# Optimization experiments

Hardware: AMD Instinct MI355X
Metric: run time of the kernel (lower is better)

The kernel has to match this reference:

```python
import jax, jax.numpy as jnp
import numpy as np

B, S, D = 1, 2048, 2048
HQ, HKV, HD = 32, 4, 128
E, K, F = 8, 2, 768
EPS = 1e-6
ROPE_THETA = 1000000.0


def rmsnorm(x, scale, eps=EPS):
    var = jnp.mean(jnp.square(x), axis=-1, keepdims=True)
    return x * jax.lax.rsqrt(var + eps) * scale


def rotate_half(x):
    h = x.shape[-1] // 2
    return jnp.concatenate([-x[..., h:], x[..., :h]], axis=-1)


def rope_cos_sin(seq_len, head_dim, dtype=jnp.float32):
    inv_freq = 1.0 / (ROPE_THETA ** (jnp.arange(0, head_dim, 2, dtype=jnp.float32) / head_dim))
    angles = jnp.arange(seq_len, dtype=jnp.float32)[:, None] * inv_freq[None, :]  # (S, HD/2)
    emb = jnp.concatenate([angles, angles], axis=-1)  # (S, HD)
    return jnp.cos(emb).astype(dtype), jnp.sin(emb).astype(dtype)


def setup_inputs() -> dict:
    key = jax.random.key(0)
    ks = jax.random.split(key, 16)
    s = lambda i, shape, scale: jax.random.normal(ks[i], shape, dtype=jnp.float32) * scale
    inp = {
        "hidden_states": s(0, (B, S, D), 1.0),
        "ln1_scale": jnp.ones((D,), jnp.float32),
        "ln2_scale": jnp.ones((D,), jnp.float32),
        "Wq": s(1, (D, HQ * HD), 0.02),
        "Wk": s(2, (D, HKV * HD), 0.02),
        "Wv": s(3, (D, HKV * HD), 0.02),
        "Wo": s(4, (HQ * HD, D), 0.02),
        "q_norm_scale": jnp.ones((HD,), jnp.float32),
        "k_norm_scale": jnp.ones((HD,), jnp.float32),
        "router_W": s(5, (D, E), 0.02),
        "up_W": s(6, (E, D, F), 0.02),
        "up_b": jnp.zeros((E, F), jnp.float32),
        "down_W": s(7, (E, F, D), 0.02),
        "down_b": jnp.zeros((E, D), jnp.float32),
    }
    return inp


def reference(hidden_states, ln1_scale, ln2_scale, Wq, Wk, Wv, Wo,
              q_norm_scale, k_norm_scale, router_W, up_W, up_b, down_W, down_b):
    b, s_len, d = hidden_states.shape
    # ---- pre-norm + self-attention ----
    residual = hidden_states
    x = rmsnorm(hidden_states, ln1_scale)
    q = (x @ Wq).reshape(b, s_len, HQ, HD)
    k = (x @ Wk).reshape(b, s_len, HKV, HD)
    v = (x @ Wv).reshape(b, s_len, HKV, HD)
    q = rmsnorm(q, q_norm_scale)
    k = rmsnorm(k, k_norm_scale)
    cos, sin = rope_cos_sin(s_len, HD, q.dtype)
    cos = cos[None, :, None, :]
    sin = sin[None, :, None, :]
    q = q * cos + rotate_half(q) * sin
    k = k * cos + rotate_half(k) * sin
    g = HQ // HKV
    k = jnp.repeat(k, g, axis=2)  # (b, s, HQ, HD)
    v = jnp.repeat(v, g, axis=2)
    scores = jnp.einsum('bqhd,bkhd->bhqk', q, k) / jnp.sqrt(jnp.asarray(HD, q.dtype))
    causal = jnp.tril(jnp.ones((s_len, s_len), bool))
    scores = jnp.where(causal[None, None], scores, jnp.asarray(-1e9, scores.dtype))
    probs = jax.nn.softmax(scores, axis=-1)
    attn = jnp.einsum('bhqk,bkhd->bqhd', probs, v).reshape(b, s_len, HQ * HD)
    attn_out = attn @ Wo
    hidden = residual + attn_out
    # ---- pre-norm + dense-all-experts MoE ----
    residual = hidden
    xf = rmsnorm(hidden, ln2_scale).reshape(-1, d)  # (T, D)
    router_logits = xf @ router_W  # (T, E)
    routing_weights = jax.nn.softmax(router_logits, axis=-1)
    gating_weights, selected = jax.lax.top_k(routing_weights, K)  # (T, K)
    gating_weights = gating_weights / jnp.sum(gating_weights, axis=-1, keepdims=True)
    expert_mask = jax.nn.one_hot(selected, E, dtype=gating_weights.dtype)  # (T, K, E)
    h = jax.nn.silu(jnp.einsum('td,edf->tef', xf, up_W) + up_b[None])  # (T, E, F)
    expert_outputs = jnp.einsum('tef,efd->ted', h, down_W) + down_b[None]  # (T, E, D)
    weighted = jnp.einsum('tke,ted->tkd', expert_mask, expert_outputs)  # (T, K, D)
    moe_out = jnp.sum(weighted * gating_weights[..., None], axis=1).reshape(b, s_len, d)
    hidden = residual + moe_out
    # ---- load balancing auxiliary loss (no attention mask path) ----
    expert_usage = jnp.mean(jnp.mean(expert_mask, axis=0), axis=0) * E  # (E,)
    su = jnp.sum(expert_usage)
    aux_loss = su * su / (E * E)
    return hidden, router_logits, aux_loss
```

## Files before the change

kernel.cpp:

```cpp
#include <hip/hip_runtime.h>
#include <cmath>

typedef __bf16 bf16_t;
typedef __bf16 bf16x8 __attribute__((ext_vector_type(8)));
typedef __bf16 bf16x4 __attribute__((ext_vector_type(4)));
typedef float  f32x4  __attribute__((ext_vector_type(4)));

#define SLEN 2048
#define DMOD 2048
#define NHQ  32
#define NHKV 4
#define HD   128
#define NQC  4096
#define NKVC 512
#define NQKVC 5120
#define NEXP 8
#define NF   768

#define KSTR 136
#define VSTR 72
#define PSTR 72

__device__ __forceinline__ float wredsum(float v) {
#pragma unroll
  for (int off = 32; off > 0; off >>= 1) v += __shfl_xor(v, off);
  return v;
}

__device__ __forceinline__ void gll16(const bf16_t* g, bf16_t* l) {
  __builtin_amdgcn_global_load_lds((const __attribute__((address_space(1))) void*)g,
                                   (__attribute__((address_space(3))) void*)l, 16, 0, 0);
}

__global__ void rope_table_k(float* __restrict__ cosT, float* __restrict__ sinT) {
  int idx = blockIdx.x * 256 + threadIdx.x;
  if (idx >= SLEN * 64) return;
  int t = idx >> 6, j = idx & 63;
  double inv = exp(-0.2158673524681918 * (double)j);
  double ang = (double)t * inv;
  cosT[idx] = (float)cos(ang);
  sinT[idx] = (float)sin(ang);
}

__global__ __launch_bounds__(256) void transpose_split2_k(const float* __restrict__ in,
                                                          bf16_t* __restrict__ outH,
                                                          bf16_t* __restrict__ outL,
                                                          int R, int C) {
  __shared__ float tile[32][33];
  int tx = threadIdx.x, ty = threadIdx.y;
  int c0 = blockIdx.x * 32, r0 = blockIdx.y * 32;
#pragma unroll
  for (int i = 0; i < 4; i++)
    tile[ty + i * 8][tx] = in[(size_t)(r0 + ty + i * 8) * C + c0 + tx];
  __syncthreads();
#pragma unroll
  for (int i = 0; i < 4; i++) {
    int c = c0 + ty + i * 8;
    int r = r0 + tx;
    float w = tile[tx][ty + i * 8];
    bf16_t hi = (bf16_t)w;
    bf16_t lo = (bf16_t)(w - (float)hi);
    size_t o = (size_t)c * R + r;
    outH[o] = hi;
    outL[o] = lo;
  }
}

__global__ __launch_bounds__(256) void transpose_plain_k(const float* __restrict__ in,
                                                         bf16_t* __restrict__ out,
                                                         int R, int C) {
  __shared__ float tile[32][33];
  int b = blockIdx.z;
  const float* inb = in + (size_t)b * R * C;
  bf16_t* outb = out + (size_t)b * R * C;
  int tx = threadIdx.x, ty = threadIdx.y;
  int c0 = blockIdx.x * 32, r0 = blockIdx.y * 32;
#pragma unroll
  for (int i = 0; i < 4; i++)
    tile[ty + i * 8][tx] = inb[(size_t)(r0 + ty + i * 8) * C + c0 + tx];
  __syncthreads();
#pragma unroll
  for (int i = 0; i < 4; i++) {
    int c = c0 + ty + i * 8;
    int r = r0 + tx;
    outb[(size_t)c * R + r] = (bf16_t)tile[tx][ty + i * 8];
  }
}

__global__ __launch_bounds__(256) void rmsnorm1_k(const float* __restrict__ hs,
                                                  const float* __restrict__ sc,
                                                  bf16_t* __restrict__ xnH,
                                                  bf16_t* __restrict__ xnL) {
  const int t = blockIdx.x;
  const float* row = hs + (size_t)t * DMOD;
  const int tid = threadIdx.x;
  const int i0 = tid * 8;
  float4 a = *(const float4*)(row + i0);
  float4 b = *(const float4*)(row + i0 + 4);
  float x[8] = {a.x, a.y, a.z, a.w, b.x, b.y, b.z, b.w};
  float ss = 0.f;
#pragma unroll
  for (int j = 0; j < 8; j++) ss += x[j] * x[j];
  ss = wredsum(ss);
  __shared__ float red[4];
  if ((tid & 63) == 0) red[tid >> 6] = ss;
  __syncthreads();
  float rn = rsqrtf((red[0] + red[1] + red[2] + red[3]) * (1.f / 2048.f) + 1e-6f);
#pragma unroll
  for (int j = 0; j < 8; j++) {
    float v = x[j] * rn * sc[i0 + j];
    bf16_t hi = (bf16_t)v;
    bf16_t lo = (bf16_t)(v - (float)hi);
    xnH[(size_t)t * DMOD + i0 + j] = hi;
    xnL[(size_t)t * DMOD + i0 + j] = lo;
  }
}

template <bool RESID>
__global__ __launch_bounds__(256, 3) void gemm_split_k(const bf16_t* __restrict__ Ah,
                                                       const bf16_t* __restrict__ Al,
                                                       int lda,
                                                       const bf16_t* __restrict__ Bh,
                                                       const bf16_t* __restrict__ Bl,
                                                       int ldb, int K,
                                                       const float* __restrict__ resid,
                                                       float* __restrict__ C, int ldc) {
  __shared__ bf16_t AsH[2][128][32], AsL[2][128][32], BsH[2][64][32], BsL[2][64][32];
  const int t = threadIdx.x;
  const int w = t >> 6, lane = t & 63;
  const int m16 = lane & 15, quad = lane >> 4;
  const int nwg = gridDim.x * gridDim.y;
  const int flat = blockIdx.y * gridDim.x + blockIdx.x;
  int tile = flat;
  if ((nwg & 7) == 0) tile = (flat & 7) * (nwg >> 3) + (flat >> 3);
  const int bx = tile % gridDim.x, by = tile / gridDim.x;
  const int m0 = by * 128, n0 = bx * 64;
  const int wm = (w & 1) * 64, wn = (w >> 1) * 32;
  f32x4 acc[4][2];
#pragma unroll
  for (int i = 0; i < 4; i++)
#pragma unroll
    for (int j = 0; j < 2; j++) acc[i][j] = (f32x4){0.f, 0.f, 0.f, 0.f};

  const int srow = t >> 2;
  const int scol = (t & 3) * 8;
  const int lw = w * 512;
  const bf16_t* gAh0 = Ah + (size_t)(m0 + srow) * lda + scol;
  const bf16_t* gAh1 = Ah + (size_t)(m0 + 64 + srow) * lda + scol;
  const bf16_t* gAl0 = Al + (size_t)(m0 + srow) * lda + scol;
  const bf16_t* gAl1 = Al + (size_t)(m0 + 64 + srow) * lda + scol;
  const bf16_t* gBh0 = Bh + (size_t)(n0 + srow) * ldb + scol;
  const bf16_t* gBl0 = Bl + (size_t)(n0 + srow) * ldb + scol;

  auto stage = [&](int buf, int k0) {
    gll16(gAh0 + k0, &AsH[buf][0][0] + lw);
    gll16(gAh1 + k0, &AsH[buf][0][0] + 2048 + lw);
    gll16(gAl0 + k0, &AsL[buf][0][0] + lw);
    gll16(gAl1 + k0, &AsL[buf][0][0] + 2048 + lw);
    gll16(gBh0 + k0, &BsH[buf][0][0] + lw);
    gll16(gBl0 + k0, &BsL[buf][0][0] + lw);
  };

  stage(0, 0);
  int cur = 0;
  for (int k0 = 32; k0 <= K; k0 += 32) {
    if (k0 < K) {
      stage(cur ^ 1, k0);
      asm volatile("s_waitcnt vmcnt(6)" ::: "memory");
    } else {
      asm volatile("s_waitcnt vmcnt(0)" ::: "memory");
    }
    __builtin_amdgcn_sched_barrier(0);
    __builtin_amdgcn_s_barrier();
    __builtin_amdgcn_sched_barrier(0);
    bf16x8 a_h[4], a_l[4];
#pragma unroll
    for (int mt = 0; mt < 4; mt++) {
      a_h[mt] = *(const bf16x8*)(&AsH[cur][wm + mt * 16 + m16][quad * 8]);
      a_l[mt] = *(const bf16x8*)(&AsL[cur][wm + mt * 16 + m16][quad * 8]);
    }
#pragma unroll
    for (int nt = 0; nt < 2; nt++) {
      bf16x8 b_h = *(const bf16x8*)(&BsH[cur][wn + nt * 16 + m16][quad * 8]);
      bf16x8 b_l = *(const bf16x8*)(&BsL[cur][wn + nt * 16 + m16][quad * 8]);
#pragma unroll
      for (int mt = 0; mt < 4; mt++) {
        acc[mt][nt] = __builtin_amdgcn_mfma_f32_16x16x32_bf16(a_h[mt], b_h, acc[mt][nt], 0, 0, 0);
        acc[mt][nt] = __builtin_amdgcn_mfma_f32_16x16x32_bf16(a_l[mt], b_h, acc[mt][nt], 0, 0, 0);
        acc[mt][nt] = __builtin_amdgcn_mfma_f32_16x16x32_bf16(a_h[mt], b_l, acc[mt][nt], 0, 0, 0);
      }
    }
    __builtin_amdgcn_sched_barrier(0);
    __builtin_amdgcn_s_barrier();
    __builtin_amdgcn_sched_barrier(0);
    cur ^= 1;
  }
#pragma unroll
  for (int mt = 0; mt < 4; mt++)
#pragma unroll
    for (int r = 0; r < 4; r++) {
      const size_t row = m0 + wm + mt * 16 + quad * 4 + r;
#pragma unroll
      for (int nt = 0; nt < 2; nt++) {
        const size_t idx = row * ldc + n0 + wn + nt * 16 + m16;
        if (RESID) C[idx] = acc[mt][nt][r] + resid[idx];
        else       C[idx] = acc[mt][nt][r];
      }
    }
}

__global__ __launch_bounds__(128) void qknorm_rope_k(float* __restrict__ qkv,
                                                     const float* __restrict__ qsc,
                                                     const float* __restrict__ ksc,
                                                     const float* __restrict__ cosT,
                                                     const float* __restrict__ sinT) {
  const int t = blockIdx.x;
  const int hh = blockIdx.y;
  const bool isq = hh < NHQ;
  float* ptr = qkv + (size_t)t * NQKVC + (isq ? hh * HD : NQC + (hh - NHQ) * HD);
  const int i = threadIdx.x;
  float x = ptr[i];
  float ss = x * x;
  ss = wredsum(ss);
  __shared__ float red2[2];
  __shared__ float xs[128];
  if ((i & 63) == 0) red2[i >> 6] = ss;
  __syncthreads();
  float rn = rsqrtf((red2[0] + red2[1]) * (1.f / 128.f) + 1e-6f);
  float xn = x * rn * (isq ? qsc[i] : ksc[i]);
  xs[i] = xn;
  __syncthreads();
  int j = i & 63;
  float c = cosT[t * 64 + j];
  float s = sinT[t * 64 + j];
  float rot = (i < 64) ? -xs[i + 64] : xs[i - 64];
  ptr[i] = xn * c + rot * s;
}

__global__ __launch_bounds__(256) void kprep_k(const float* __restrict__ qkv,
                                               bf16_t* __restrict__ Kh,
                                               bf16_t* __restrict__ Kl) {
  const int gid = blockIdx.x * 256 + threadIdx.x;
  const int tok = gid >> 6;
  const int c = (gid & 63) * 8;
  const int hk = c >> 7, d = c & 127;
  const float* p = qkv + (size_t)tok * NQKVC + NQC + c;
  float4 a = *(const float4*)p;
  float4 b = *(const float4*)(p + 4);
  float xv[8] = {a.x, a.y, a.z, a.w, b.x, b.y, b.z, b.w};
  bf16x8 hv, lv;
#pragma unroll
  for (int j = 0; j < 8; j++) {
    bf16_t hi = (bf16_t)xv[j];
    hv[j] = hi;
    lv[j] = (bf16_t)(xv[j] - (float)hi);
  }
  const size_t o = ((size_t)hk * SLEN + tok) * HD + d;
  *(bf16x8*)(Kh + o) = hv;
  *(bf16x8*)(Kl + o) = lv;
}

__global__ __launch_bounds__(256) void vprep_k(const float* __restrict__ qkv,
                                               bf16_t* __restrict__ Vh,
                                               bf16_t* __restrict__ Vl) {
  __shared__ float tile[32][33];
  const int hk = blockIdx.z;
  const int tx = threadIdx.x, ty = threadIdx.y;
  const int t0 = blockIdx.x * 32, d0 = blockIdx.y * 32;
#pragma unroll
  for (int i = 0; i < 4; i++)
    tile[ty + i * 8][tx] =
        qkv[(size_t)(t0 + ty + i * 8) * NQKVC + NQC + NKVC + hk * HD + d0 + tx];
  __syncthreads();
#pragma unroll
  for (int i = 0; i < 4; i++) {
    int d = d0 + ty + i * 8;
    int tk = t0 + tx;
    float wv = tile[tx][ty + i * 8];
    bf16_t hi = (bf16_t)wv;
    size_t o = ((size_t)hk * HD + d) * SLEN + tk;
    Vh[o] = hi;
    Vl[o] = (bf16_t)(wv - (float)hi);
  }
}

__global__ __launch_bounds__(256) void attn_mfma_k(const float* __restrict__ qkv,
                                                   const bf16_t* __restrict__ Kph,
                                                   const bf16_t* __restrict__ Kpl,
                                                   const bf16_t* __restrict__ Vph,
                                                   const bf16_t* __restrict__ Vpl,
                                                   bf16_t* __restrict__ attnH,
                                                   bf16_t* __restrict__ attnL) {
  const int bx = blockIdx.x;
  const int hh = blockIdx.y;
  const int hk = hh >> 3;
  __shared__ bf16_t sK[2][64][KSTR];
  __shared__ bf16_t sV[2][128][VSTR];
  const int t = threadIdx.x;
  const int w = t >> 6, lane = t & 63;
  const int m16 = lane & 15, quad = lane >> 4;
  const float SCALE = 0.08838834764831845f;

  const int ksr = t >> 4;
  const int ksc = (t & 15) * 8;
  const int vsd = t >> 3;
  const int vsk = (t & 7) * 8;
  const bf16_t* KbH = Kph + (size_t)hk * SLEN * HD;
  const bf16_t* KbL = Kpl + (size_t)hk * SLEN * HD;
  const bf16_t* VbH = Vph + (size_t)hk * HD * SLEN;
  const bf16_t* VbL = Vpl + (size_t)hk * HD * SLEN;
  bf16_t* sP = &sK[0][0][0];

  for (int half = 0; half < 2; half++) {
    const int qb = half ? bx : 31 - bx;
    const int qg = qb * 64 + w * 16 + m16;

    bf16x8 Qh[4], Ql[4];
    {
      const int qrow = qb * 64 + w * 16 + m16;
      const float* qp = qkv + (size_t)qrow * NQKVC + hh * HD + quad * 8;
#pragma unroll
      for (int kc = 0; kc < 4; kc++) {
        float4 x0 = *(const float4*)(qp + kc * 32);
        float4 x1 = *(const float4*)(qp + kc * 32 + 4);
        float xv[8] = {x0.x, x0.y, x0.z, x0.w, x1.x, x1.y, x1.z, x1.w};
#pragma unroll
        for (int j = 0; j < 8; j++) {
          bf16_t hi = (bf16_t)xv[j];
          Qh[kc][j] = hi;
          Ql[kc][j] = (bf16_t)(xv[j] - (float)hi);
        }
      }
    }
    f32x4 acc[8];
#pragma unroll
    for (int i = 0; i < 8; i++) acc[i] = (f32x4){0.f, 0.f, 0.f, 0.f};
    float mrow = -1e30f, lrow = 0.f;

    for (int kb = 0; kb <= qb; kb++) {
      __syncthreads();
      {
#pragma unroll
        for (int i = 0; i < 4; i++) {
          const int row = ksr + i * 16;
          const size_t go = (size_t)(kb * 64 + row) * HD + ksc;
          *(bf16x8*)(&sK[0][row][ksc]) = *(const bf16x8*)(KbH + go);
          *(bf16x8*)(&sK[1][row][ksc]) = *(const bf16x8*)(KbL + go);
        }
      }
      {
#pragma unroll
        for (int i = 0; i < 4; i++) {
          const int d = vsd + i * 32;
          const size_t go = (size_t)d * SLEN + kb * 64 + vsk;
          *(bf16x8*)(&sV[0][d][vsk]) = *(const bf16x8*)(VbH + go);
          *(bf16x8*)(&sV[1][d][vsk]) = *(const bf16x8*)(VbL + go);
        }
      }
      __syncthreads();
      f32x4 xs[4];
#pragma unroll
      for (int nt = 0; nt < 4; nt++) {
        f32x4 s = (f32x4){0.f, 0.f, 0.f, 0.f};
        if (kb < qb || nt <= w) {
#pragma unroll
          for (int kc = 0; kc < 4; kc++) {
            bf16x8 kh = *(const bf16x8*)(&sK[0][nt * 16 + m16][kc * 32 + quad * 8]);
            bf16x8 kl = *(const bf16x8*)(&sK[1][nt * 16 + m16][kc * 32 + quad * 8]);
            s = __builtin_amdgcn_mfma_f32_16x16x32_bf16(kh, Qh[kc], s, 0, 0, 0);
            s = __builtin_amdgcn_mfma_f32_16x16x32_bf16(kh, Ql[kc], s, 0, 0, 0);
            s = __builtin_amdgcn_mfma_f32_16x16x32_bf16(kl, Qh[kc], s, 0, 0, 0);
          }
        }
        xs[nt] = s;
      }
      __syncthreads();
      float xr[4][4], p[4][4];
      float mx = -1e30f;
#pragma unroll
      for (int nt = 0; nt < 4; nt++)
#pragma unroll
        for (int r = 0; r < 4; r++) {
          int kvg = kb * 64 + nt * 16 + quad * 4 + r;
          float v = (kvg <= qg) ? xs[nt][r] * SCALE : -1e30f;
          xr[nt][r] = v;
          mx = fmaxf(mx, v);
        }
      mx = fmaxf(mx, __shfl_xor(mx, 16));
      mx = fmaxf(mx, __shfl_xor(mx, 32));
      float mn = fmaxf(mrow, mx);
      float al = __expf(mrow - mn);
      float rs = 0.f;
#pragma unroll
      for (int nt = 0; nt < 4; nt++)
#pragma unroll
        for (int r = 0; r < 4; r++) {
          float pv = __expf(xr[nt][r] - mn);
          p[nt][r] = pv;
          rs += pv;
        }
      rs += __shfl_xor(rs, 16);
      rs += __shfl_xor(rs, 32);
      lrow = lrow * al + rs;
      mrow = mn;
#pragma unroll
      for (int dt = 0; dt < 8; dt++)
#pragma unroll
        for (int r = 0; r < 4; r++) acc[dt][r] *= al;
      {
        bf16_t* base = sP + (size_t)w * 2 * 16 * PSTR;
#pragma unroll
        for (int nt = 0; nt < 4; nt++) {
          bf16x4 hv, lv;
#pragma unroll
          for (int r = 0; r < 4; r++) {
            float pv = p[nt][r];
            bf16_t hi = (bf16_t)pv;
            hv[r] = hi;
            lv[r] = (bf16_t)(pv - (float)hi);
          }
          *(bf16x4*)(base + m16 * PSTR + nt * 16 + quad * 4) = hv;
          *(bf16x4*)(base + 16 * PSTR + m16 * PSTR + nt * 16 + quad * 4) = lv;
        }
      }
      {
        const bf16_t* base = sP + (size_t)w * 2 * 16 * PSTR;
        bf16x8 Ph[2], Pl[2];
#pragma unroll
        for (int kc = 0; kc < 2; kc++) {
          Ph[kc] = *(const bf16x8*)(base + m16 * PSTR + kc * 32 + quad * 8);
          Pl[kc] = *(const bf16x8*)(base + 16 * PSTR + m16 * PSTR + kc * 32 + quad * 8);
        }
#pragma unroll
        for (int dt = 0; dt < 8; dt++)
#pragma unroll
          for (int kc = 0; kc < 2; kc++) {
            bf16x8 vh = *(const bf16x8*)(&sV[0][dt * 16 + m16][kc * 32 + quad * 8]);
            bf16x8 vl = *(const bf16x8*)(&sV[1][dt * 16 + m16][kc * 32 + quad * 8]);
            acc[dt] = __builtin_amdgcn_mfma_f32_16x16x32_bf16(vh, Ph[kc], acc[dt], 0, 0, 0);
            acc[dt] = __builtin_amdgcn_mfma_f32_16x16x32_bf16(vh, Pl[kc], acc[dt], 0, 0, 0);
            acc[dt] = __builtin_amdgcn_mfma_f32_16x16x32_bf16(vl, Ph[kc], acc[dt], 0, 0, 0);
          }
      }
    }
    __syncthreads();
    float* tb = (float*)(&sK[0][0][0]) + (size_t)w * 2048;
    const float linv = 1.f / lrow;
#pragma unroll
    for (int dt = 0; dt < 8; dt++) {
      f32x4 v = acc[dt];
#pragma unroll
      for (int r = 0; r < 4; r++) v[r] *= linv;
      *(f32x4*)(tb + m16 * 128 + dt * 16 + quad * 4) = v;
    }
    __syncthreads();
    {
      const int qr = lane >> 2, c0 = (lane & 3) * 32;
      const int tok = qb * 64 + w * 16 + qr;
      const size_t ro = (size_t)tok * NQC + hh * HD + c0;
#pragma unroll
      for (int j = 0; j < 4; j++) {
        float4 a = *(const float4*)(tb + qr * 128 + c0 + j * 8);
        float4 b = *(const float4*)(tb + qr * 128 + c0 + j * 8 + 4);
        float xv[8] = {a.x, a.y, a.z, a.w, b.x, b.y, b.z, b.w};
        bf16x8 hv, lv;
#pragma unroll
        for (int jj = 0; jj < 8; jj++) {
          bf16_t hi = (bf16_t)xv[jj];
          hv[jj] = hi;
          lv[jj] = (bf16_t)(xv[jj] - (float)hi);
        }
        *(bf16x8*)(attnH + ro + j * 8) = hv;
        *(bf16x8*)(attnL + ro + j * 8) = lv;
      }
    }
  }
}

__global__ __launch_bounds__(256) void rmsnorm2_router_k(const float* __restrict__ hid,
                                                         const float* __restrict__ sc2,
                                                         const float* __restrict__ rW,
                                                         bf16_t* __restrict__ xf,
                                                         float* __restrict__ rlog) {
  const int t = blockIdx.x;
  const float* row = hid + (size_t)t * DMOD;
  const int tid = threadIdx.x;
  const int i0 = tid * 8;
  float4 a = *(const float4*)(row + i0);
  float4 b = *(const float4*)(row + i0 + 4);
  float x[8] = {a.x, a.y, a.z, a.w, b.x, b.y, b.z, b.w};
  float ss = 0.f;
#pragma unroll
  for (int j = 0; j < 8; j++) ss += x[j] * x[j];
  ss = wredsum(ss);
  __shared__ float red[4];
  if ((tid & 63) == 0) red[tid >> 6] = ss;
  __syncthreads();
  float rn = rsqrtf((red[0] + red[1] + red[2] + red[3]) * (1.f / 2048.f) + 1e-6f);
  float acc[8];
#pragma unroll
  for (int e = 0; e < 8; e++) acc[e] = 0.f;
#pragma unroll
  for (int j = 0; j < 8; j++) {
    float xn = x[j] * rn * sc2[i0 + j];
    xf[(size_t)t * DMOD + i0 + j] = (bf16_t)xn;
    const float* w = rW + (size_t)(i0 + j) * NEXP;
#pragma unroll
    for (int e = 0; e < 8; e++) acc[e] += xn * w[e];
  }
#pragma unroll
  for (int e = 0; e < 8; e++) acc[e] = wredsum(acc[e]);
  __shared__ float wacc[4][8];
  if ((tid & 63) == 0)
#pragma unroll
    for (int e = 0; e < 8; e++) wacc[tid >> 6][e] = acc[e];
  __syncthreads();
  if (tid < 8) rlog[t * NEXP + tid] = wacc[0][tid] + wacc[1][tid] + wacc[2][tid] + wacc[3][tid];
}

__global__ void topk_k(const float* __restrict__ rlog, int* __restrict__ sel,
                       float* __restrict__ gates, float* __restrict__ aux) {
  int t = blockIdx.x * 256 + threadIdx.x;
  if (t == 0) aux[0] = 1.0f;
  if (t >= SLEN) return;
  const float* l = rlog + t * NEXP;
  int i1 = 0; float v1 = l[0];
#pragma unroll
  for (int e = 1; e < 8; e++) if (l[e] > v1) { v1 = l[e]; i1 = e; }
  int i2 = -1; float v2 = -1e30f;
#pragma unroll
  for (int e = 0; e < 8; e++) if (e != i1 && l[e] > v2) { v2 = l[e]; i2 = e; }
  float e21 = expf(v2 - v1);
  float inv = 1.f / (1.f + e21);
  sel[t * 2 + 0] = i1;
  sel[t * 2 + 1] = i2;
  gates[t * 2 + 0] = inv;
  gates[t * 2 + 1] = e21 * inv;
}

__global__ void scatter_k(const int* __restrict__ sel, const float* __restrict__ gates,
                          int* __restrict__ cnt, int* __restrict__ tok,
                          float* __restrict__ gateL, int* __restrict__ posOf) {
  int i = blockIdx.x * 256 + threadIdx.x;
  if (i >= SLEN * 2) return;
  int e = sel[i];
  int pos = atomicAdd(&cnt[e], 1);
  tok[e * SLEN + pos] = i >> 1;
  gateL[e * SLEN + pos] = gates[i];
  posOf[i] = pos;
}

__global__ void prefix_k(const int* __restrict__ cnt, int* __restrict__ baseP) {
  if (threadIdx.x == 0) {
    int b = 0;
#pragma unroll
    for (int e = 0; e < 8; e++) { baseP[e] = b; b += cnt[e]; }
  }
}

__global__ __launch_bounds__(256, 5) void gemm_up_k(const bf16_t* __restrict__ xf,
                                                    const bf16_t* __restrict__ upWT,
                                                    const int* __restrict__ cnt,
                                                    const int* __restrict__ tok,
                                                    const float* __restrict__ up_b,
                                                    bf16_t* __restrict__ hbuf) {
  const int e = blockIdx.z;
  const int c = cnt[e];
  const int m0 = blockIdx.y * 128;
  if (m0 >= c) return;
  const int n0 = blockIdx.x * 64;
  __shared__ bf16_t As[2][128][32], Bs[2][64][32];
  const int t = threadIdx.x;
  const int w = t >> 6, lane = t & 63;
  const int m16 = lane & 15, quad = lane >> 4;
  const int wm = (w & 1) * 64, wn = (w >> 1) * 32;
  const int srow = t >> 2, scol = (t & 3) * 8;
  const int lw = w * 512;
  const int* tokE = tok + e * SLEN;
  int r0 = m0 + srow;      if (r0 >= c) r0 = c - 1;
  int r1 = m0 + 64 + srow; if (r1 >= c) r1 = c - 1;
  const bf16_t* ga0 = xf + (size_t)tokE[r0] * DMOD + scol;
  const bf16_t* ga1 = xf + (size_t)tokE[r1] * DMOD + scol;
  const bf16_t* gb0 = upWT + (size_t)e * NF * DMOD + (size_t)(n0 + srow) * DMOD + scol;
  f32x4 acc[4][2];
#pragma unroll
  for (int i = 0; i < 4; i++)
#pragma unroll
    for (int j = 0; j < 2; j++) acc[i][j] = (f32x4){0.f, 0.f, 0.f, 0.f};

  auto stage = [&](int buf, int k0) {
    gll16(ga0 + k0, &As[buf][0][0] + lw);
    gll16(ga1 + k0, &As[buf][0][0] + 2048 + lw);
    gll16(gb0 + k0, &Bs[buf][0][0] + lw);
  };

  stage(0, 0);
  int cur = 0;
  for (int k0 = 32; k0 <= DMOD; k0 += 32) {
    if (k0 < DMOD) {
      stage(cur ^ 1, k0);
      asm volatile("s_waitcnt vmcnt(3)" ::: "memory");
    } else {
      asm volatile("s_waitcnt vmcnt(0)" ::: "memory");
    }
    __builtin_amdgcn_sched_barrier(0);
    __builtin_amdgcn_s_barrier();
    __builtin_amdgcn_sched_barrier(0);
    bf16x8 a[4];
#pragma unroll
    for (int mt = 0; mt < 4; mt++)
      a[mt] = *(const bf16x8*)(&As[cur][wm + mt * 16 + m16][quad * 8]);
#pragma unroll
    for (int nt = 0; nt < 2; nt++) {
      bf16x8 b = *(const bf16x8*)(&Bs[cur][wn + nt * 16 + m16][quad * 8]);
#pragma unroll
      for (int mt = 0; mt < 4; mt++)
        acc[mt][nt] = __builtin_amdgcn_mfma_f32_16x16x32_bf16(a[mt], b, acc[mt][nt], 0, 0, 0);
    }
    __builtin_amdgcn_sched_barrier(0);
    __builtin_amdgcn_s_barrier();
    __builtin_amdgcn_sched_barrier(0);
    cur ^= 1;
  }
#pragma unroll
  for (int mt = 0; mt < 4; mt++)
#pragma unroll
    for (int r = 0; r < 4; r++) {
      int slot = m0 + wm + mt * 16 + quad * 4 + r;
      if (slot < c) {
#pragma unroll
        for (int nt = 0; nt < 2; nt++) {
          int n = n0 + wn + nt * 16 + m16;
          float x = acc[mt][nt][r] + up_b[e * NF + n];
          float v = x / (1.f + __expf(-x));
          hbuf[((size_t)e * SLEN + slot) * NF + n] = (bf16_t)v;
        }
      }
    }
}

__global__ __launch_bounds__(256, 5) void gemm_down_k(const bf16_t* __restrict__ hbuf,
                                                      const bf16_t* __restrict__ downWT,
                                                      const int* __restrict__ cnt,
                                                      const float* __restrict__ gateL,
                                                      const float* __restrict__ down_b,
                                                      const int* __restrict__ baseP,
                                                      float* __restrict__ dbuf) {
  const int e = blockIdx.z;
  const int c = cnt[e];
  const int m0 = blockIdx.y * 128;
  if (m0 >= c) return;
  const int n0 = blockIdx.x * 64;
  __shared__ bf16_t As[2][128][32], Bs[2][64][32];
  const int t = threadIdx.x;
  const int w = t >> 6, lane = t & 63;
  const int m16 = lane & 15, quad = lane >> 4;
  const int wm = (w & 1) * 64, wn = (w >> 1) * 32;
  const int srow = t >> 2, scol = (t & 3) * 8;
  const int lw = w * 512;
  const bf16_t* Ab = hbuf + (size_t)e * SLEN * NF;
  const bf16_t* ga0 = Ab + (size_t)(m0 + srow) * NF + scol;
  const bf16_t* ga1 = Ab + (size_t)(m0 + 64 + srow) * NF + scol;
  const bf16_t* gb0 = downWT + (size_t)e * DMOD * NF + (size_t)(n0 + srow) * NF + scol;
  f32x4 acc[4][2];
#pragma unroll
  for (int i = 0; i < 4; i++)
#pragma unroll
    for (int j = 0; j < 2; j++) acc[i][j] = (f32x4){0.f, 0.f, 0.f, 0.f};

  auto stage = [&](int buf, int k0) {
    gll16(ga0 + k0, &As[buf][0][0] + lw);
    gll16(ga1 + k0, &As[buf][0][0] + 2048 + lw);
    gll16(gb0 + k0, &Bs[buf][0][0] + lw);
  };

  stage(0, 0);
  int cur = 0;
  for (int k0 = 32; k0 <= NF; k0 += 32) {
    if (k0 < NF) {
      stage(cur ^ 1, k0);
      asm volatile("s_waitcnt vmcnt(3)" ::: "memory");
    } else {
      asm volatile("s_waitcnt vmcnt(0)" ::: "memory");
    }
    __builtin_amdgcn_sched_barrier(0);
    __builtin_amdgcn_s_barrier();
    __builtin_amdgcn_sched_barrier(0);
    bf16x8 a[4];
#pragma unroll
    for (int mt = 0; mt < 4; mt++)
      a[mt] = *(const bf16x8*)(&As[cur][wm + mt * 16 + m16][quad * 8]);
#pragma unroll
    for (int nt = 0; nt < 2; nt++) {
      bf16x8 b = *(const bf16x8*)(&Bs[cur][wn + nt * 16 + m16][quad * 8]);
#pragma unroll
      for (int mt = 0; mt < 4; mt++)
        acc[mt][nt] = __builtin_amdgcn_mfma_f32_16x16x32_bf16(a[mt], b, acc[mt][nt], 0, 0, 0);
    }
    __builtin_amdgcn_sched_barrier(0);
    __builtin_amdgcn_s_barrier();
    __builtin_amdgcn_sched_barrier(0);
    cur ^= 1;
  }
  const int eb = baseP[e];
#pragma unroll
  for (int mt = 0; mt < 4; mt++)
#pragma unroll
    for (int r = 0; r < 4; r++) {
      int slot = m0 + wm + mt * 16 + quad * 4 + r;
      if (slot < c) {
        float g = gateL[e * SLEN + slot];
#pragma unroll
        for (int nt = 0; nt < 2; nt++) {
          int n = n0 + wn + nt * 16 + m16;
          dbuf[(size_t)(eb + slot) * DMOD + n] = g * (acc[mt][nt][r] + down_b[e * DMOD + n]);
        }
      }
    }
}

__global__ __launch_bounds__(256) void combine_k(const float* __restrict__ dbuf,
                                                 const int* __restrict__ sel,
                                                 const int* __restrict__ posOf,
                                                 const int* __restrict__ baseP,
                                                 float* __restrict__ dout) {
  const int t = blockIdx.x;
  const int i0 = threadIdx.x * 8;
  const int r0 = baseP[sel[t * 2 + 0]] + posOf[t * 2 + 0];
  const int r1 = baseP[sel[t * 2 + 1]] + posOf[t * 2 + 1];
  const float* a = dbuf + (size_t)r0 * DMOD + i0;
  const float* b = dbuf + (size_t)r1 * DMOD + i0;
  float* o = dout + (size_t)t * DMOD + i0;
  float4 o0 = *(const float4*)o,       o1 = *(const float4*)(o + 4);
  float4 a0 = *(const float4*)a,       a1 = *(const float4*)(a + 4);
  float4 b0 = *(const float4*)b,       b1 = *(const float4*)(b + 4);
  o0.x += a0.x + b0.x; o0.y += a0.y + b0.y; o0.z += a0.z + b0.z; o0.w += a0.w + b0.w;
  o1.x += a1.x + b1.x; o1.y += a1.y + b1.y; o1.z += a1.z + b1.z; o1.w += a1.w + b1.w;
  *(float4*)o = o0;
  *(float4*)(o + 4) = o1;
}

extern "C" void kernel_launch(void* const* d_in, const int* in_sizes, int n_in,
                              void* d_out, int out_size, void* d_ws, size_t ws_size,
                              hipStream_t stream) {
  (void)in_sizes; (void)n_in; (void)out_size;
  const float* hs   = (const float*)d_in[0];
  const float* ln1  = (const float*)d_in[1];
  const float* ln2  = (const float*)d_in[2];
  const float* Wq   = (const float*)d_in[3];
  const float* Wk   = (const float*)d_in[4];
  const float* Wv   = (const float*)d_in[5];
  const float* Wo   = (const float*)d_in[6];
  const float* qns  = (const float*)d_in[7];
  const float* kns  = (const float*)d_in[8];
  const float* rW   = (const float*)d_in[9];
  const float* upW  = (const float*)d_in[10];
  const float* upB  = (const float*)d_in[11];
  const float* dnW  = (const float*)d_in[12];
  const float* dnB  = (const float*)d_in[13];
  float* dout = (float*)d_out;

  const size_t NEED = 135431168ull;
  if (ws_size < NEED) return;
  char* ws = (char*)d_ws;
  const size_t OA = 0;
  const size_t OB = OA + 41943040ull;
  const size_t OC = OB + 33554432ull;
  const size_t OD = OC + 16777216ull;
  const size_t OE = OD + 41943040ull;

  bf16_t* BqkvH  = (bf16_t*)(ws + OA);
  bf16_t* BqkvL  = (bf16_t*)(ws + OA + 20971520ull);
  bf16_t* attnH  = (bf16_t*)(ws + OA);
  bf16_t* attnL  = (bf16_t*)(ws + OA + 16777216ull);
  bf16_t* Kph    = (bf16_t*)(ws + OA + 33554432ull);
  bf16_t* Kpl    = Kph + 1048576;
  bf16_t* Vph    = Kpl + 1048576;
  bf16_t* Vpl    = Vph + 1048576;
  bf16_t* upWT   = (bf16_t*)(ws + OA);
  float*  dbuf   = (float*)(ws + OA);
  bf16_t* WoH    = (bf16_t*)(ws + OB);
  bf16_t* WoL    = (bf16_t*)(ws + OB + 16777216ull);
  bf16_t* hbuf   = (bf16_t*)(ws + OB);
  bf16_t* xnH    = (bf16_t*)(ws + OC);
  bf16_t* xnL    = (bf16_t*)(ws + OC + 8388608ull);
  bf16_t* xf     = (bf16_t*)(ws + OC);
  float*  qkv    = (float*)(ws + OD);
  bf16_t* downWT = (bf16_t*)(ws + OD);
  float*  cosT   = (float*)(ws + OE);
  float*  sinT   = (float*)(ws + OE + 524288ull);
  int*    sel    = (int*)(ws + OE + 1048576ull);
  float*  gates  = (float*)(ws + OE + 1064960ull);
  int*    cnt    = (int*)(ws + OE + 1081344ull);
  int*    tok    = (int*)(ws + OE + 1082368ull);
  float*  gateL  = (float*)(ws + OE + 1147904ull);
  int*    posOf  = (int*)(ws + OE + 1213440ull);
  int*    baseP  = (int*)(ws + OE + 1229824ull);

  hipMemsetAsync(cnt, 0, 1024, stream);
  rope_table_k<<<512, 256, 0, stream>>>(cosT, sinT);

  dim3 tb(32, 8);
  transpose_split2_k<<<dim3(128, 64), tb, 0, stream>>>(Wq, BqkvH, BqkvL, 2048, 4096);
  transpose_split2_k<<<dim3(16, 64), tb, 0, stream>>>(Wk, BqkvH + (size_t)4096 * 2048,
                                                      BqkvL + (size_t)4096 * 2048, 2048, 512);
  transpose_split2_k<<<dim3(16, 64), tb, 0, stream>>>(Wv, BqkvH + (size_t)4608 * 2048,
                                                      BqkvL + (size_t)4608 * 2048, 2048, 512);
  transpose_split2_k<<<dim3(64, 128), tb, 0, stream>>>(Wo, WoH, WoL, 4096, 2048);

  rmsnorm1_k<<<2048, 256, 0, stream>>>(hs, ln1, xnH, xnL);
  gemm_split_k<false><<<dim3(80, 16), 256, 0, stream>>>(xnH, xnL, 2048, BqkvH, BqkvL,
                                                        2048, 2048, nullptr, qkv, NQKVC);
  qknorm_rope_k<<<dim3(2048, 36), 128, 0, stream>>>(qkv, qns, kns, cosT, sinT);
  kprep_k<<<512, 256, 0, stream>>>(qkv, Kph, Kpl);
  vprep_k<<<dim3(64, 4, 4), tb, 0, stream>>>(qkv, Vph, Vpl);
  attn_mfma_k<<<dim3(16, 32), 256, 0, stream>>>(qkv, Kph, Kpl, Vph, Vpl, attnH, attnL);
  gemm_split_k<true><<<dim3(32, 16), 256, 0, stream>>>(attnH, attnL, 4096, WoH, WoL,
                                                       4096, 4096, hs, dout, DMOD);

  rmsnorm2_router_k<<<2048, 256, 0, stream>>>(dout, ln2, rW, xf, dout + 4194304);
  topk_k<<<8, 256, 0, stream>>>(dout + 4194304, sel, gates, dout + 4210688);
  scatter_k<<<16, 256, 0, stream>>>(sel, gates, cnt, tok, gateL, posOf);
  prefix_k<<<1, 64, 0, stream>>>(cnt, baseP);

  transpose_plain_k<<<dim3(24, 64, 8), tb, 0, stream>>>(upW, upWT, 2048, 768);
  transpose_plain_k<<<dim3(64, 24, 8), tb, 0, stream>>>(dnW, downWT, 768, 2048);

  gemm_up_k<<<dim3(12, 16, 8), 256, 0, stream>>>(xf, upWT, cnt, tok, upB, hbuf);
  gemm_down_k<<<dim3(32, 16, 8), 256, 0, stream>>>(hbuf, downWT, cnt, gateL, dnB, baseP, dbuf);
  combine_k<<<2048, 256, 0, stream>>>(dbuf, sel, posOf, baseP, dout);
}
```

Measured before the change: 848.4 us.

## Rewrite split-bf16 GEMM as 8-wave 128x128 tiles with 4-stage prefetch pipeline

Replaces the 4-wave 128x64 split-precision GEMM with an 8-wave 512-thread kernel covering 128x128 output tiles. Shared-memory staging goes from double buffering to a four-slot ring with three stages prefetched ahead, using graded vmcnt waits. MFMA blocks are wrapped in s_setprio so math waves get priority over loads. This raises reuse of each staged tile and hides global latency better, at the cost of more LDS per block (128 KB), lower occupancy, and half as many workgroups for the Wo projection (256 blocks).

New measurement: 907.4 us. +6.9%, slower.

```diff
diff --git a/kernel.cpp b/kernel.cpp
--- a/kernel.cpp
+++ b/kernel.cpp
@@ -117,15 +117,15 @@
 }
 
 template <bool RESID>
-__global__ __launch_bounds__(256, 3) void gemm_split_k(const bf16_t* __restrict__ Ah,
-                                                       const bf16_t* __restrict__ Al,
-                                                       int lda,
-                                                       const bf16_t* __restrict__ Bh,
-                                                       const bf16_t* __restrict__ Bl,
-                                                       int ldb, int K,
-                                                       const float* __restrict__ resid,
-                                                       float* __restrict__ C, int ldc) {
-  __shared__ bf16_t AsH[2][128][32], AsL[2][128][32], BsH[2][64][32], BsL[2][64][32];
+__global__ __launch_bounds__(512, 2) void gemm8_k(const bf16_t* __restrict__ Ah,
+                                                  const bf16_t* __restrict__ Al,
+                                                  int lda,
+                                                  const bf16_t* __restrict__ Bh,
+                                                  const bf16_t* __restrict__ Bl,
+                                                  int ldb, int K,
+                                                  const float* __restrict__ resid,
+                                                  float* __restrict__ C, int ldc) {
+  __shared__ bf16_t AsH[4][128][32], AsL[4][128][32], BsH[4][128][32], BsL[4][128][32];
   const int t = threadIdx.x;
   const int w = t >> 6, lane = t & 63;
   const int m16 = lane & 15, quad = lane >> 4;
@@ -134,7 +134,7 @@
   int tile = flat;
   if ((nwg & 7) == 0) tile = (flat & 7) * (nwg >> 3) + (flat >> 3);
   const int bx = tile % gridDim.x, by = tile / gridDim.x;
-  const int m0 = by * 128, n0 = bx * 64;
+  const int m0 = by * 128, n0 = bx * 128;
   const int wm = (w & 1) * 64, wn = (w >> 1) * 32;
   f32x4 acc[4][2];
 #pragma unroll
@@ -142,58 +142,62 @@
 #pragma unroll
     for (int j = 0; j < 2; j++) acc[i][j] = (f32x4){0.f, 0.f, 0.f, 0.f};
 
-  const int srow = t >> 2;
-  const int scol = (t & 3) * 8;
-  const int lw = w * 512;
-  const bf16_t* gAh0 = Ah + (size_t)(m0 + srow) * lda + scol;
-  const bf16_t* gAh1 = Ah + (size_t)(m0 + 64 + srow) * lda + scol;
-  const bf16_t* gAl0 = Al + (size_t)(m0 + srow) * lda + scol;
-  const bf16_t* gAl1 = Al + (size_t)(m0 + 64 + srow) * lda + scol;
-  const bf16_t* gBh0 = Bh + (size_t)(n0 + srow) * ldb + scol;
-  const bf16_t* gBl0 = Bl + (size_t)(n0 + srow) * ldb + scol;
-
-  auto stage = [&](int buf, int k0) {
-    gll16(gAh0 + k0, &AsH[buf][0][0] + lw);
-    gll16(gAh1 + k0, &AsH[buf][0][0] + 2048 + lw);
-    gll16(gAl0 + k0, &AsL[buf][0][0] + lw);
-    gll16(gAl1 + k0, &AsL[buf][0][0] + 2048 + lw);
-    gll16(gBh0 + k0, &BsH[buf][0][0] + lw);
-    gll16(gBl0 + k0, &BsL[buf][0][0] + lw);
+  const int sr = w * 16 + (lane >> 2);
+  const int sc = (lane & 3) * 8;
+  const bf16_t* gAh = Ah + (size_t)(m0 + sr) * lda + sc;
+  const bf16_t* gAl = Al + (size_t)(m0 + sr) * lda + sc;
+  const bf16_t* gBh = Bh + (size_t)(n0 + sr) * ldb + sc;
+  const bf16_t* gBl = Bl + (size_t)(n0 + sr) * ldb + sc;
+
+  const int NH = K >> 5;
+  auto stage = [&](int h) {
+    const int slot = h & 3;
+    const int k0 = h * 32;
+    gll16(gAh + k0, &AsH[slot][w * 16][0]);
+    gll16(gAl + k0, &AsL[slot][w * 16][0]);
+    gll16(gBh + k0, &BsH[slot][w * 16][0]);
+    gll16(gBl + k0, &BsL[slot][w * 16][0]);
   };
 
-  stage(0, 0);
-  int cur = 0;
-  for (int k0 = 32; k0 <= K; k0 += 32) {
-    if (k0 < K) {
-      stage(cur ^ 1, k0);
-      asm volatile("s_waitcnt vmcnt(6)" ::: "memory");
-    } else {
-      asm volatile("s_waitcnt vmcnt(0)" ::: "memory");
-    }
+  stage(0);
+  stage(1);
+  stage(2);
+  for (int h = 0; h < NH; h++) {
+    if (h + 3 < NH) stage(h + 3);
+    const int rem = NH - 1 - h;
+    if (rem >= 3)      asm volatile("s_waitcnt vmcnt(12)" ::: "memory");
+    else if (rem == 2) asm volatile("s_waitcnt vmcnt(8)" ::: "memory");
+    else if (rem == 1) asm volatile("s_waitcnt vmcnt(4)" ::: "memory");
+    else               asm volatile("s_waitcnt vmcnt(0)" ::: "memory");
     __builtin_amdgcn_sched_barrier(0);
     __builtin_amdgcn_s_barrier();
     __builtin_amdgcn_sched_barrier(0);
+    const int slot = h & 3;
     bf16x8 a_h[4], a_l[4];
 #pragma unroll
     for (int mt = 0; mt < 4; mt++) {
-      a_h[mt] = *(const bf16x8*)(&AsH[cur][wm + mt * 16 + m16][quad * 8]);
-      a_l[mt] = *(const bf16x8*)(&AsL[cur][wm + mt * 16 + m16][quad * 8]);
-    }
+      a_h[mt] = *(const bf16x8*)(&AsH[slot][wm + mt * 16 + m16][quad * 8]);
+      a_l[mt] = *(const bf16x8*)(&AsL[slot][wm + mt * 16 + m16][quad * 8]);
+    }
+    bf16x8 b_h[2], b_l[2];
 #pragma unroll
     for (int nt = 0; nt < 2; nt++) {
-      bf16x8 b_h = *(const bf16x8*)(&BsH[cur][wn + nt * 16 + m16][quad * 8]);
-      bf16x8 b_l = *(const bf16x8*)(&BsL[cur][wn + nt * 16 + m16][quad * 8]);
+      b_h[nt] = *(const bf16x8*)(&BsH[slot][wn + nt * 16 + m16][quad * 8]);
+      b_l[nt] = *(const bf16x8*)(&BsL[slot][wn + nt * 16 + m16][quad * 8]);
+    }
+    __builtin_amdgcn_s_setprio(1);
+#pragma unroll
+    for (int nt = 0; nt < 2; nt++)
 #pragma unroll
       for (int mt = 0; mt < 4; mt++) {
-        acc[mt][nt] = __builtin_amdgcn_mfma_f32_16x16x32_bf16(a_h[mt], b_h, acc[mt][nt], 0, 0, 0);
-        acc[mt][nt] = __builtin_amdgcn_mfma_f32_16x16x32_bf16(a_l[mt], b_h, acc[mt][nt], 0, 0, 0);
-        acc[mt][nt] = __builtin_amdgcn_mfma_f32_16x16x32_bf16(a_h[mt], b_l, acc[mt][nt], 0, 0, 0);
-      }
-    }
+        acc[mt][nt] = __builtin_amdgcn_mfma_f32_16x16x32_bf16(a_h[mt], b_h[nt], acc[mt][nt], 0, 0, 0);
+        acc[mt][nt] = __builtin_amdgcn_mfma_f32_16x16x32_bf16(a_l[mt], b_h[nt], acc[mt][nt], 0, 0, 0);
+        acc[mt][nt] = __builtin_amdgcn_mfma_f32_16x16x32_bf16(a_h[mt], b_l[nt], acc[mt][nt], 0, 0, 0);
+      }
+    __builtin_amdgcn_s_setprio(0);
     __builtin_amdgcn_sched_barrier(0);
     __builtin_amdgcn_s_barrier();
     __builtin_amdgcn_sched_barrier(0);
-    cur ^= 1;
   }
 #pragma unroll
   for (int mt = 0; mt < 4; mt++)
@@ -809,14 +813,14 @@
   transpose_split2_k<<<dim3(64, 128), tb, 0, stream>>>(Wo, WoH, WoL, 4096, 2048);
 
   rmsnorm1_k<<<2048, 256, 0, stream>>>(hs, ln1, xnH, xnL);
-  gemm_split_k<false><<<dim3(80, 16), 256, 0, stream>>>(xnH, xnL, 2048, BqkvH, BqkvL,
-                                                        2048, 2048, nullptr, qkv, NQKVC);
+  gemm8_k<false><<<dim3(40, 16), 512, 0, stream>>>(xnH, xnL, 2048, BqkvH, BqkvL,
+                                                   2048, 2048, nullptr, qkv, NQKVC);
   qknorm_rope_k<<<dim3(2048, 36), 128, 0, stream>>>(qkv, qns, kns, cosT, sinT);
   kprep_k<<<512, 256, 0, stream>>>(qkv, Kph, Kpl);
   vprep_k<<<dim3(64, 4, 4), tb, 0, stream>>>(qkv, Vph, Vpl);
   attn_mfma_k<<<dim3(16, 32), 256, 0, stream>>>(qkv, Kph, Kpl, Vph, Vpl, attnH, attnL);
-  gemm_split_k<true><<<dim3(32, 16), 256, 0, stream>>>(attnH, attnL, 4096, WoH, WoL,
-                                                       4096, 4096, hs, dout, DMOD);
+  gemm8_k<true><<<dim3(16, 16), 512, 0, stream>>>(attnH, attnL, 4096, WoH, WoL,
+                                                  4096, 4096, hs, dout, DMOD);
 
   rmsnorm2_router_k<<<2048, 256, 0, stream>>>(dout, ln2, rW, xf, dout + 4194304);
   topk_k<<<8, 256, 0, stream>>>(dout + 4194304, sel, gates, dout + 4210688);
```
